# Kernel tuning notes

Hardware: AMD Instinct MI355X
Metric: run time of the kernel (lower is better)

## Reference

```python
import jax, jax.numpy as jnp
import numpy as np
import math

EMBED_DIM = 1024
NUM_HEADS = 16
HEAD_DIM = EMBED_DIM // NUM_HEADS
CQ = 256  # chunksize_q
CK = 256  # chunksize_k
L = 2048
B = 4


def setup_inputs() -> dict:
    key = jax.random.key(0)
    ks = jax.random.split(key, 7)
    E = EMBED_DIM
    # xavier_uniform bound for (3E, E): sqrt(6/(3E+E))
    bound = math.sqrt(6.0 / (3 * E + E))
    in_proj_weight = jax.random.uniform(ks[3], (3 * E, E), jnp.float32, -bound, bound)
    in_proj_bias = jnp.zeros((3 * E,), jnp.float32)
    # nn.Linear default init (kaiming uniform ~ U(-1/sqrt(E), 1/sqrt(E)))
    wb = 1.0 / math.sqrt(E)
    out_w = jax.random.uniform(ks[4], (E, E), jnp.float32, -wb, wb)
    out_b = jnp.zeros((E,), jnp.float32)
    return {
        "q": jax.random.normal(ks[0], (L, B, E), jnp.float32),
        "k": jax.random.normal(ks[1], (L, B, E), jnp.float32),
        "v": jax.random.normal(ks[2], (L, B, E), jnp.float32),
        "in_proj_weight": in_proj_weight,
        "in_proj_bias": in_proj_bias,
        "out_w": out_w,
        "out_b": out_b,
    }


def _chunked_attention(q, k, v):
    # q: (BH, Lq, d), k/v: (BH, Lk, d). Online-softmax over k-chunks,
    # vectorized over the chunk grid (same math as the python loops).
    BH, Lq, d = q.shape
    Lk = k.shape[1]
    nq, nk = Lq // CQ, Lk // CK
    q = q / math.sqrt(HEAD_DIM)
    qc = q.reshape(BH, nq, CQ, d)
    kc = k.reshape(BH, nk, CK, d)
    vc = v.reshape(BH, nk, CK, d)
    # scores per (q-chunk, k-chunk) pair: (BH, nq, nk, CQ, CK)
    s = jnp.einsum('bqid,bkjd->bqkij', qc, kc)
    m = jax.lax.stop_gradient(jnp.max(s, axis=-1, keepdims=True))  # detached chunk max
    e = jnp.exp(s - m)
    row_sum = e.sum(axis=-1)                                # (BH, nq, nk, CQ)
    vals = jnp.einsum('bqkij,bkjd->bqkid', e, vc)           # (BH, nq, nk, CQ, d)
    m = m[..., 0]                                           # (BH, nq, nk, CQ)
    gmax = jnp.max(m, axis=2, keepdims=True)                # global max over k-chunks
    diff = jnp.exp(m - gmax)
    all_vals = (vals * diff[..., None]).sum(axis=2)         # (BH, nq, CQ, d)
    all_w = (row_sum * diff).sum(axis=2)[..., None]         # (BH, nq, CQ, 1)
    out = all_vals / all_w
    return out.reshape(BH, Lq, d)


def reference(q, k, v, in_proj_weight, in_proj_bias, out_w, out_b):
    E, H, hd = EMBED_DIM, NUM_HEADS, HEAD_DIM
    l, b, _ = q.shape
    lk = k.shape[0]
    w_q, w_k, w_v = jnp.split(in_proj_weight, 3, axis=0)
    b_q, b_k, b_v = jnp.split(in_proj_bias, 3, axis=0)
    qp = q @ w_q.T + b_q
    kp = k @ w_k.T + b_k
    vp = v @ w_v.T + b_v
    # (L, B, E) -> (B*H, L, hd)
    qp = qp.reshape(l, b * H, hd).transpose(1, 0, 2)
    kp = kp.reshape(lk, b * H, hd).transpose(1, 0, 2)
    vp = vp.reshape(lk, b * H, hd).transpose(1, 0, 2)
    attn = _chunked_attention(qp, kp, vp)                   # (B*H, L, hd)
    attn = attn.transpose(1, 0, 2).reshape(l, b, E)
    return attn @ out_w.T + out_b
```

## Files before the change

### kernel.cpp

```cpp
#include <hip/hip_runtime.h>

typedef unsigned short u16;
typedef short bf16x8 __attribute__((ext_vector_type(8)));
typedef float f32x4 __attribute__((ext_vector_type(4)));
typedef unsigned u32x2 __attribute__((ext_vector_type(2)));

#define MFMA16(a, b, c) __builtin_amdgcn_mfma_f32_16x16x32_bf16(a, b, c, 0, 0, 0)

static constexpr int L_ = 2048, B_ = 4, E_ = 1024, H_ = 16, HD_ = 64;
static constexpr int M_ = L_ * B_;
static constexpr int BH_ = B_ * H_;
static constexpr size_t NA = (size_t)M_ * E_;
#define QSCALE 0.18033688f

__device__ __forceinline__ void gload16(const void* g, void* l) {
  __builtin_amdgcn_global_load_lds((const __attribute__((address_space(1))) void*)g,
                                   (__attribute__((address_space(3))) void*)l, 16, 0, 0);
}

__device__ __forceinline__ u16 f2bf(float f) {
  union { float f; unsigned u; } v; v.f = f;
  unsigned r = v.u + 0x7fffu + ((v.u >> 16) & 1u);
  return (u16)(r >> 16);
}

__device__ __forceinline__ unsigned pkbf(float a, float b) {
#if __has_builtin(__builtin_amdgcn_cvt_pk_bf16_f32)
  auto r = __builtin_amdgcn_cvt_pk_bf16_f32(a, b);
  unsigned u; __builtin_memcpy(&u, &r, 4); return u;
#else
  return (unsigned)f2bf(a) | ((unsigned)f2bf(b) << 16);
#endif
}

__device__ __forceinline__ float fexp2(float x) {
#if __has_builtin(__builtin_amdgcn_exp2f)
  return __builtin_amdgcn_exp2f(x);
#else
  return exp2f(x);
#endif
}

__global__ __launch_bounds__(256) void cvt_all(
    const float* __restrict__ q, const float* __restrict__ k, const float* __restrict__ v,
    const float* __restrict__ w, const float* __restrict__ ow,
    u16* __restrict__ qb, u16* __restrict__ kb, u16* __restrict__ vb,
    u16* __restrict__ wbf, u16* __restrict__ owbf) {
  const size_t idx = ((size_t)blockIdx.x * 256 + threadIdx.x) * 8;
  const float* s; u16* d; size_t off;
  if (idx < NA) { s = q; d = qb; off = idx; }
  else if (idx < 2 * NA) { s = k; d = kb; off = idx - NA; }
  else if (idx < 3 * NA) { s = v; d = vb; off = idx - 2 * NA; }
  else if (idx < 3 * NA + (size_t)3 * E_ * E_) { s = w; d = wbf; off = idx - 3 * NA; }
  else { s = ow; d = owbf; off = idx - 3 * NA - (size_t)3 * E_ * E_; }
  const float4 a = *(const float4*)(s + off);
  const float4 b = *(const float4*)(s + off + 4);
  uint4 r;
  r.x = pkbf(a.x, a.y); r.y = pkbf(a.z, a.w);
  r.z = pkbf(b.x, b.y); r.w = pkbf(b.z, b.w);
  *(uint4*)(d + off) = r;
}

__global__ __launch_bounds__(256) void gemm_qkv(
    const u16* __restrict__ Aq, const u16* __restrict__ Ak, const u16* __restrict__ Av,
    const u16* __restrict__ Wbf, const float* __restrict__ bias,
    u16* __restrict__ oq, u16* __restrict__ ok, u16* __restrict__ ov) {
  __shared__ __align__(16) u16 As[128][32];
  __shared__ __align__(16) u16 Bs[128][32];
  const int t = threadIdx.x, wave = t >> 6, lane = t & 63, quad = lane >> 4, l15 = lane & 15;
  const int n0 = blockIdx.x * 128, m0 = blockIdx.y * 128, z = blockIdx.z;
  const u16* A = (z == 0) ? Aq : (z == 1 ? Ak : Av);
  const u16* Wz = Wbf + (size_t)z * E_ * E_;
  const float* bz = bias + z * E_;
  const int wm = (wave >> 1) * 64, wn = (wave & 1) * 64;

  const f32x4 vzero = {0.f, 0.f, 0.f, 0.f};
  f32x4 acc[4][4];
#pragma unroll
  for (int i = 0; i < 4; ++i)
#pragma unroll
    for (int j = 0; j < 4; ++j) acc[i][j] = vzero;

  for (int kk = 0; kk < E_; kk += 32) {
#pragma unroll
    for (int i = 0; i < 2; ++i) {
      const int c0 = (i * 4 + wave) * 64;
      const int c = c0 + lane;
      const int r = c >> 2;
      const int p = (c & 3) ^ ((r >> 1) & 3);
      gload16(A + (size_t)(m0 + r) * E_ + kk + p * 8, (u16*)As + c0 * 8);
      gload16(Wz + (size_t)(n0 + r) * E_ + kk + p * 8, (u16*)Bs + c0 * 8);
    }
    __syncthreads();
    bf16x8 af[4], bfr[4];
#pragma unroll
    for (int x = 0; x < 4; ++x) {
      const int ra = wm + x * 16 + l15;
      af[x] = *(const bf16x8*)&As[ra][(quad ^ ((ra >> 1) & 3)) * 8];
      const int rb = wn + x * 16 + l15;
      bfr[x] = *(const bf16x8*)&Bs[rb][(quad ^ ((rb >> 1) & 3)) * 8];
    }
#pragma unroll
    for (int mi = 0; mi < 4; ++mi)
#pragma unroll
      for (int ni = 0; ni < 4; ++ni)
        acc[mi][ni] = MFMA16(af[mi], bfr[ni], acc[mi][ni]);
    __syncthreads();
  }

#pragma unroll
  for (int ni = 0; ni < 4; ++ni) {
    const int n = n0 + wn + ni * 16 + l15;
    const float bv = bz[n];
#pragma unroll
    for (int mi = 0; mi < 4; ++mi) {
#pragma unroll
      for (int r = 0; r < 4; ++r) {
        const int m = m0 + wm + mi * 16 + quad * 4 + r;
        const float val = acc[mi][ni][r] + bv;
        const int l = m >> 2, bb = m & 3, h = n >> 6, d = n & 63;
        const int s = bb * H_ + h;
        if (z == 0) {
          oq[(size_t)s * (L_ * HD_) + (size_t)l * HD_ + d] = f2bf(val * QSCALE);
        } else if (z == 1) {
          ok[(size_t)s * (L_ * HD_) + (size_t)l * HD_ + d] = f2bf(val);
        } else {
          ov[((size_t)s * HD_ + d) * L_ + l] = f2bf(val);
        }
      }
    }
  }
}

__global__ __launch_bounds__(256) void gemm_out(
    const u16* __restrict__ A, const u16* __restrict__ Wbf,
    const float* __restrict__ bias, float* __restrict__ out) {
  __shared__ __align__(16) u16 As[128][32];
  __shared__ __align__(16) u16 Bs[128][32];
  const int t = threadIdx.x, wave = t >> 6, lane = t & 63, quad = lane >> 4, l15 = lane & 15;
  const int n0 = blockIdx.x * 128, m0 = blockIdx.y * 128;
  const int wm = (wave >> 1) * 64, wn = (wave & 1) * 64;

  const f32x4 vzero = {0.f, 0.f, 0.f, 0.f};
  f32x4 acc[4][4];
#pragma unroll
  for (int i = 0; i < 4; ++i)
#pragma unroll
    for (int j = 0; j < 4; ++j) acc[i][j] = vzero;

  for (int kk = 0; kk < E_; kk += 32) {
#pragma unroll
    for (int i = 0; i < 2; ++i) {
      const int c0 = (i * 4 + wave) * 64;
      const int c = c0 + lane;
      const int r = c >> 2;
      const int p = (c & 3) ^ ((r >> 1) & 3);
      gload16(A + (size_t)(m0 + r) * E_ + kk + p * 8, (u16*)As + c0 * 8);
      gload16(Wbf + (size_t)(n0 + r) * E_ + kk + p * 8, (u16*)Bs + c0 * 8);
    }
    __syncthreads();
    bf16x8 af[4], bfr[4];
#pragma unroll
    for (int x = 0; x < 4; ++x) {
      const int ra = wm + x * 16 + l15;
      af[x] = *(const bf16x8*)&As[ra][(quad ^ ((ra >> 1) & 3)) * 8];
      const int rb = wn + x * 16 + l15;
      bfr[x] = *(const bf16x8*)&Bs[rb][(quad ^ ((rb >> 1) & 3)) * 8];
    }
#pragma unroll
    for (int mi = 0; mi < 4; ++mi)
#pragma unroll
      for (int ni = 0; ni < 4; ++ni)
        acc[mi][ni] = MFMA16(af[mi], bfr[ni], acc[mi][ni]);
    __syncthreads();
  }

#pragma unroll
  for (int ni = 0; ni < 4; ++ni) {
    const int n = n0 + wn + ni * 16 + l15;
    const float bv = bias[n];
#pragma unroll
    for (int mi = 0; mi < 4; ++mi) {
#pragma unroll
      for (int r = 0; r < 4; ++r) {
        const int m = m0 + wm + mi * 16 + quad * 4 + r;
        out[(size_t)m * E_ + n] = acc[mi][ni][r] + bv;
      }
    }
  }
}

__global__ __launch_bounds__(256, 4) void attn_fused(
    const u16* __restrict__ Q, const u16* __restrict__ K,
    const u16* __restrict__ Vt, u16* __restrict__ O) {
  __shared__ __align__(16) u16 Ks[128][64];
  __shared__ __align__(16) u16 Vs[64][128];
  const int t = threadIdx.x, wave = t >> 6, lane = t & 63, quad = lane >> 4, l15 = lane & 15;
  const int bh = blockIdx.y, q0 = blockIdx.x * 64;
  const u16* Qb = Q + (size_t)bh * L_ * HD_;
  const u16* Kb = K + (size_t)bh * L_ * HD_;
  const u16* Vb = Vt + (size_t)bh * HD_ * L_;
  u16* Pw = (u16*)Ks + wave * 2048;

  const int qrow = q0 + wave * 16 + l15;
  const bf16x8 qf0 = *(const bf16x8*)(Qb + (size_t)qrow * HD_ + quad * 8);
  const bf16x8 qf1 = *(const bf16x8*)(Qb + (size_t)qrow * HD_ + 32 + quad * 8);

  const f32x4 vzero = {0.f, 0.f, 0.f, 0.f};
  float run_l = 0.f;
  f32x4 oacc[4];
#pragma unroll
  for (int di = 0; di < 4; ++di) oacc[di] = vzero;

  const int sigma = (l15 & 7) ^ ((l15 >> 2) & 2);
  u16* Pwb = Pw + l15 * 128 + (quad & 1) * 4;
  const int qh = quad >> 1;

  for (int j0 = 0; j0 < L_; j0 += 128) {
#pragma unroll
    for (int i = 0; i < 4; ++i) {
      const int c0 = (i * 4 + wave) * 64;
      const int c = c0 + lane;
      {
        const int r = c >> 3, p = (c & 7) ^ (r & 7);
        gload16(Kb + (size_t)(j0 + r) * HD_ + p * 8, (u16*)Ks + c0 * 8);
      }
      {
        const int r = c >> 4, p = (c & 15) ^ (r & 15);
        gload16(Vb + (size_t)r * L_ + j0 + p * 8, (u16*)Vs + c0 * 8);
      }
    }
    __syncthreads();

    f32x4 sacc[8];
#pragma unroll
    for (int ni = 0; ni < 8; ++ni) sacc[ni] = vzero;
    __builtin_amdgcn_s_setprio(1);
#pragma unroll
    for (int ni = 0; ni < 8; ++ni) {
      const int row = ni * 16 + l15;
      const bf16x8 k0 = *(const bf16x8*)&Ks[row][(quad ^ (row & 7)) * 8];
      const bf16x8 k1 = *(const bf16x8*)&Ks[row][((4 + quad) ^ (row & 7)) * 8];
      sacc[ni] = MFMA16(k0, qf0, sacc[ni]);
      sacc[ni] = MFMA16(k1, qf1, sacc[ni]);
    }
    __builtin_amdgcn_s_setprio(0);

    __syncthreads();

#pragma unroll
    for (int ni = 0; ni < 8; ++ni) {
      const float p0 = fexp2(sacc[ni][0]);
      const float p1 = fexp2(sacc[ni][1]);
      const float p2 = fexp2(sacc[ni][2]);
      const float p3 = fexp2(sacc[ni][3]);
      run_l += (p0 + p1) + (p2 + p3);
      u32x2 pv;
      pv.x = pkbf(p0, p1);
      pv.y = pkbf(p2, p3);
      *(u32x2*)(Pwb + (((2 * ni + qh) ^ sigma) << 3)) = pv;
    }

    {
      __builtin_amdgcn_s_setprio(1);
#pragma unroll
      for (int s2 = 0; s2 < 4; ++s2) {
        const bf16x8 pa = *(const bf16x8*)(Pw + l15 * 128 + (((s2 * 4 + quad) ^ sigma) << 3));
#pragma unroll
        for (int di = 0; di < 4; ++di) {
          const int row = di * 16 + l15;
          const bf16x8 vb = *(const bf16x8*)&Vs[row][((s2 * 4 + quad) ^ (row & 15)) * 8];
          oacc[di] = MFMA16(pa, vb, oacc[di]);
        }
      }
      __builtin_amdgcn_s_setprio(0);
    }
    __syncthreads();
  }

  run_l += __shfl_xor(run_l, 16);
  run_l += __shfl_xor(run_l, 32);
  const int b = bh >> 4, h = bh & 15;
#pragma unroll
  for (int r = 0; r < 4; ++r) {
    const float rs = __shfl(run_l, quad * 4 + r);
    const float inv = 1.f / rs;
    const int l = q0 + wave * 16 + quad * 4 + r;
#pragma unroll
    for (int di = 0; di < 4; ++di) {
      const int e = h * 64 + di * 16 + l15;
      O[((size_t)l * B_ + b) * E_ + e] = f2bf(oacc[di][r] * inv);
    }
  }
}

extern "C" void kernel_launch(void* const* d_in, const int* in_sizes, int n_in,
                              void* d_out, int out_size, void* d_ws, size_t ws_size,
                              hipStream_t stream) {
  const float* q = (const float*)d_in[0];
  const float* k = (const float*)d_in[1];
  const float* v = (const float*)d_in[2];
  const float* w = (const float*)d_in[3];
  const float* bqkv = (const float*)d_in[4];
  const float* ow = (const float*)d_in[5];
  const float* ob = (const float*)d_in[6];

  u16* qb = (u16*)d_ws;
  u16* kb = qb + NA;
  u16* vb = kb + NA;
  u16* qs = vb + NA;
  u16* ks = qs + NA;
  u16* vt = ks + NA;
  u16* wbf = vt + NA;
  u16* owbf = wbf + (size_t)3 * E_ * E_;
  u16* obuf = qb;

  cvt_all<<<dim3(14336), 256, 0, stream>>>(q, k, v, w, ow, qb, kb, vb, wbf, owbf);
  gemm_qkv<<<dim3(E_ / 128, M_ / 128, 3), 256, 0, stream>>>(qb, kb, vb, wbf, bqkv, qs, ks, vt);
  attn_fused<<<dim3(L_ / 64, BH_), 256, 0, stream>>>(qs, ks, vt, obuf);
  gemm_out<<<dim3(E_ / 128, M_ / 128), 256, 0, stream>>>(obuf, owbf, ob, (float*)d_out);
}
```

Measured before the change: 388.6 us.

## Use two waves per attention block with 32 query rows each and XCD-aware remap

```diff
diff --git a/kernel.cpp b/kernel.cpp
--- a/kernel.cpp
+++ b/kernel.cpp
@@ -190,27 +190,35 @@
   }
 }
 
-__global__ __launch_bounds__(256, 4) void attn_fused(
+__global__ __launch_bounds__(128, 3) void attn_fused(
     const u16* __restrict__ Q, const u16* __restrict__ K,
     const u16* __restrict__ Vt, u16* __restrict__ O) {
   __shared__ __align__(16) u16 Ks[128][64];
   __shared__ __align__(16) u16 Vs[64][128];
   const int t = threadIdx.x, wave = t >> 6, lane = t & 63, quad = lane >> 4, l15 = lane & 15;
-  const int bh = blockIdx.y, q0 = blockIdx.x * 64;
+  const int id = blockIdx.y * 32 + blockIdx.x;
+  const int nid = (id & 7) * 256 + (id >> 3);
+  const int bh = nid >> 5, q0 = (nid & 31) * 64;
   const u16* Qb = Q + (size_t)bh * L_ * HD_;
   const u16* Kb = K + (size_t)bh * L_ * HD_;
   const u16* Vb = Vt + (size_t)bh * HD_ * L_;
-  u16* Pw = (u16*)Ks + wave * 2048;
-
-  const int qrow = q0 + wave * 16 + l15;
-  const bf16x8 qf0 = *(const bf16x8*)(Qb + (size_t)qrow * HD_ + quad * 8);
-  const bf16x8 qf1 = *(const bf16x8*)(Qb + (size_t)qrow * HD_ + 32 + quad * 8);
+  u16* Pw = (u16*)Ks + wave * 4096;
+
+  bf16x8 qf[2][2];
+#pragma unroll
+  for (int g = 0; g < 2; ++g) {
+    const int qrow = q0 + wave * 32 + g * 16 + l15;
+    qf[g][0] = *(const bf16x8*)(Qb + (size_t)qrow * HD_ + quad * 8);
+    qf[g][1] = *(const bf16x8*)(Qb + (size_t)qrow * HD_ + 32 + quad * 8);
+  }
 
   const f32x4 vzero = {0.f, 0.f, 0.f, 0.f};
-  float run_l = 0.f;
-  f32x4 oacc[4];
-#pragma unroll
-  for (int di = 0; di < 4; ++di) oacc[di] = vzero;
+  float run_l[2] = {0.f, 0.f};
+  f32x4 oacc[2][4];
+#pragma unroll
+  for (int g = 0; g < 2; ++g)
+#pragma unroll
+    for (int di = 0; di < 4; ++di) oacc[g][di] = vzero;
 
   const int sigma = (l15 & 7) ^ ((l15 >> 2) & 2);
   u16* Pwb = Pw + l15 * 128 + (quad & 1) * 4;
@@ -218,8 +226,8 @@
 
   for (int j0 = 0; j0 < L_; j0 += 128) {
 #pragma unroll
-    for (int i = 0; i < 4; ++i) {
-      const int c0 = (i * 4 + wave) * 64;
+    for (int i = 0; i < 8; ++i) {
+      const int c0 = (i * 2 + wave) * 64;
       const int c = c0 + lane;
       {
         const int r = c >> 3, p = (c & 7) ^ (r & 7);
@@ -232,45 +240,55 @@
     }
     __syncthreads();
 
-    f32x4 sacc[8];
-#pragma unroll
-    for (int ni = 0; ni < 8; ++ni) sacc[ni] = vzero;
+    f32x4 sacc[2][8];
+#pragma unroll
+    for (int g = 0; g < 2; ++g)
+#pragma unroll
+      for (int ni = 0; ni < 8; ++ni) sacc[g][ni] = vzero;
     __builtin_amdgcn_s_setprio(1);
 #pragma unroll
     for (int ni = 0; ni < 8; ++ni) {
       const int row = ni * 16 + l15;
       const bf16x8 k0 = *(const bf16x8*)&Ks[row][(quad ^ (row & 7)) * 8];
       const bf16x8 k1 = *(const bf16x8*)&Ks[row][((4 + quad) ^ (row & 7)) * 8];
-      sacc[ni] = MFMA16(k0, qf0, sacc[ni]);
-      sacc[ni] = MFMA16(k1, qf1, sacc[ni]);
+      sacc[0][ni] = MFMA16(k0, qf[0][0], sacc[0][ni]);
+      sacc[0][ni] = MFMA16(k1, qf[0][1], sacc[0][ni]);
+      sacc[1][ni] = MFMA16(k0, qf[1][0], sacc[1][ni]);
+      sacc[1][ni] = MFMA16(k1, qf[1][1], sacc[1][ni]);
     }
     __builtin_amdgcn_s_setprio(0);
 
     __syncthreads();
 
 #pragma unroll
-    for (int ni = 0; ni < 8; ++ni) {
-      const float p0 = fexp2(sacc[ni][0]);
-      const float p1 = fexp2(sacc[ni][1]);
-      const float p2 = fexp2(sacc[ni][2]);
-      const float p3 = fexp2(sacc[ni][3]);
-      run_l += (p0 + p1) + (p2 + p3);
-      u32x2 pv;
-      pv.x = pkbf(p0, p1);
-      pv.y = pkbf(p2, p3);
-      *(u32x2*)(Pwb + (((2 * ni + qh) ^ sigma) << 3)) = pv;
+    for (int g = 0; g < 2; ++g) {
+#pragma unroll
+      for (int ni = 0; ni < 8; ++ni) {
+        const float p0 = fexp2(sacc[g][ni][0]);
+        const float p1 = fexp2(sacc[g][ni][1]);
+        const float p2 = fexp2(sacc[g][ni][2]);
+        const float p3 = fexp2(sacc[g][ni][3]);
+        run_l[g] += (p0 + p1) + (p2 + p3);
+        u32x2 pv;
+        pv.x = pkbf(p0, p1);
+        pv.y = pkbf(p2, p3);
+        *(u32x2*)(Pwb + g * 2048 + (((2 * ni + qh) ^ sigma) << 3)) = pv;
+      }
     }
 
     {
       __builtin_amdgcn_s_setprio(1);
 #pragma unroll
       for (int s2 = 0; s2 < 4; ++s2) {
-        const bf16x8 pa = *(const bf16x8*)(Pw + l15 * 128 + (((s2 * 4 + quad) ^ sigma) << 3));
+        const int go = (((s2 * 4 + quad) ^ sigma) << 3);
+        const bf16x8 pa0 = *(const bf16x8*)(Pw + l15 * 128 + go);
+        const bf16x8 pa1 = *(const bf16x8*)(Pw + 2048 + l15 * 128 + go);
 #pragma unroll
         for (int di = 0; di < 4; ++di) {
           const int row = di * 16 + l15;
           const bf16x8 vb = *(const bf16x8*)&Vs[row][((s2 * 4 + quad) ^ (row & 15)) * 8];
-          oacc[di] = MFMA16(pa, vb, oacc[di]);
+          oacc[0][di] = MFMA16(pa0, vb, oacc[0][di]);
+          oacc[1][di] = MFMA16(pa1, vb, oacc[1][di]);
         }
       }
       __builtin_amdgcn_s_setprio(0);
@@ -278,18 +296,22 @@
     __syncthreads();
   }
 
-  run_l += __shfl_xor(run_l, 16);
-  run_l += __shfl_xor(run_l, 32);
   const int b = bh >> 4, h = bh & 15;
 #pragma unroll
-  for (int r = 0; r < 4; ++r) {
-    const float rs = __shfl(run_l, quad * 4 + r);
-    const float inv = 1.f / rs;
-    const int l = q0 + wave * 16 + quad * 4 + r;
-#pragma unroll
-    for (int di = 0; di < 4; ++di) {
-      const int e = h * 64 + di * 16 + l15;
-      O[((size_t)l * B_ + b) * E_ + e] = f2bf(oacc[di][r] * inv);
+  for (int g = 0; g < 2; ++g) {
+    float s = run_l[g];
+    s += __shfl_xor(s, 16);
+    s += __shfl_xor(s, 32);
+#pragma unroll
+    for (int r = 0; r < 4; ++r) {
+      const float rs = __shfl(s, quad * 4 + r);
+      const float inv = 1.f / rs;
+      const int l = q0 + wave * 32 + g * 16 + quad * 4 + r;
+#pragma unroll
+      for (int di = 0; di < 4; ++di) {
+        const int e = h * 64 + di * 16 + l15;
+        O[((size_t)l * B_ + b) * E_ + e] = f2bf(oacc[g][di][r] * inv);
+      }
     }
   }
 }
@@ -317,6 +339,6 @@
 
   cvt_all<<<dim3(14336), 256, 0, stream>>>(q, k, v, w, ow, qb, kb, vb, wbf, owbf);
   gemm_qkv<<<dim3(E_ / 128, M_ / 128, 3), 256, 0, stream>>>(qb, kb, vb, wbf, bqkv, qs, ks, vt);
-  attn_fused<<<dim3(L_ / 64, BH_), 256, 0, stream>>>(qs, ks, vt, obuf);
+  attn_fused<<<dim3(32, BH_), 128, 0, stream>>>(qs, ks, vt, obuf);
   gemm_out<<<dim3(E_ / 128, M_ / 128), 256, 0, stream>>>(obuf, owbf, ob, (float*)d_out);
 }
```

Measured after the change: 577.3 us. +48.5%, slower.
